# Kernel tuning notes

Measured on AMD Instinct MI355X. Metric: run time of the kernel, lower is better.

Reference implementation:

```python
import jax, jax.numpy as jnp
import numpy as np

B, C, H, W = 4, 16, 512, 512
OUT = 16
HID = 64
EPS = 1e-5


def _ln(x, g, b):
    mu = x.mean(-1, keepdims=True)
    v = x.var(-1, keepdims=True)
    return (x - mu) / jnp.sqrt(v + EPS) * g + b


def setup_inputs() -> dict:
    key = jax.random.key(0)
    ks = jax.random.split(key, 8)
    HW = H * W
    d = {}
    d['input'] = jax.random.normal(ks[0], (B, C, H, W), jnp.float32)
    d['W1'] = jax.random.normal(ks[1], (HID, HW), jnp.float32) * 0.01   # Linear1 weight [64, HW]
    d['b1'] = jnp.zeros((HID,), jnp.float32)
    d['ln1_g'] = jnp.ones((HID,), jnp.float32)
    d['ln1_b'] = jnp.zeros((HID,), jnp.float32)
    d['W2'] = jax.random.normal(ks[2], (HW, HID), jnp.float32) * 0.02   # Linear2 weight [HW, 64]
    d['b2'] = jnp.zeros((HW,), jnp.float32)
    d['ln2_g'] = jnp.ones((HW,), jnp.float32)
    d['ln2_b'] = jnp.zeros((HW,), jnp.float32)
    d['cw1'] = jax.random.normal(ks[3], (1, C, 1, 1), jnp.float32) * 0.1   # 1x1 conv C->1
    d['cb1'] = jnp.zeros((1,), jnp.float32)
    d['cw3'] = jax.random.normal(ks[4], (OUT, C, 3, 3), jnp.float32) * 0.05  # 3x3 conv C->OUT
    d['cb3'] = jnp.zeros((OUT,), jnp.float32)
    d['bn_g'] = jnp.ones((OUT,), jnp.float32)
    d['bn_b'] = jnp.zeros((OUT,), jnp.float32)
    return d


def reference(input, W1, b1, ln1_g, ln1_b, W2, b2, ln2_g, ln2_b, cw1, cb1, cw3, cb3, bn_g, bn_b):
    Bq, Cq, Hq, Wq = input.shape
    HW = Hq * Wq
    m = input.reshape(Bq, Cq, HW)
    # Linear1 -> LN -> ReLU  (per-channel over flattened spatial dim)
    h = jax.nn.relu(_ln(m @ W1.T + b1, ln1_g, ln1_b))            # [B, C, 64]
    # Linear2 -> LN -> ReLU
    m2 = jax.nn.relu(_ln(h @ W2.T + b2, ln2_g, ln2_b))           # [B, C, HW]
    m2 = m2.reshape(Bq, Cq, Hq, Wq)
    # 1x1 conv C -> 1
    score = jnp.einsum('bchw,oc->bohw', m2, cw1[:, :, 0, 0]) + cb1[:, None, None]  # [B,1,H,W]
    # keep_topk: ratio 0.25, no grad
    K = HW // 4
    flat = jax.lax.stop_gradient(score.reshape(Bq, HW))
    _, idx = jax.lax.top_k(flat, K)                               # [B, K]
    mask = jnp.zeros_like(flat).at[jnp.arange(Bq)[:, None], idx].set(1.0).reshape(Bq, 1, Hq, Wq)
    # boolean-mask gather: torch selects in ascending flat-index order
    idx_s = jnp.sort(idx, axis=1)                                 # [B, K]
    g = jnp.take_along_axis(m, idx_s[:, None, :], axis=2).reshape(Bq, Cq, Hq // 2, Wq // 2)
    # out_conv: 3x3 conv -> BatchNorm (batch stats, training mode) -> ReLU
    y = jax.lax.conv_general_dilated(g, cw3, (1, 1), [(1, 1), (1, 1)],
                                     dimension_numbers=('NCHW', 'OIHW', 'NCHW'))
    y = y + cb3[:, None, None]
    mu = y.mean((0, 2, 3), keepdims=True)
    v = y.var((0, 2, 3), keepdims=True)
    y = jax.nn.relu((y - mu) / jnp.sqrt(v + EPS) * bn_g[:, None, None] + bn_b[:, None, None])
    return (y, mask)
```

## Files before the change

### kernel.cpp

```cpp
#include <hip/hip_runtime.h>

#define HWN    262144
#define KSEL   65536
#define TIECAP 2048

#define OFF_H      0
#define OFF_DOT1   32768
#define OFF_G      65536
#define OFF_WBAR   98304
#define OFF_WB     98816
#define OFF_SB     99328
#define OFF_MU2    99360
#define OFF_ISIG2  99872
#define OFF_STATE  100384
#define OFF_HIST   100448
#define OFF_TIECNT 116832
#define OFF_CHCNT  116848
#define OFF_TIELST 116864
#define OFF_CHLST  149632
#define OFF_BCNT   182400
#define OFF_BOFF   186496
#define OFF_BNP    190592
#define OFF_BNC    452736
#define OFF_PART2  458752
#define OFF_HT     1015808
#define REGION2    1048576

__device__ __forceinline__ unsigned monokey(double s){
  unsigned long long b = (unsigned long long)__double_as_longlong(s);
  b = (b & 0x8000000000000000ULL) ? ~b : (b | 0x8000000000000000ULL);
  return (unsigned)(b >> 32);
}

__global__ void k_zero(unsigned* hist, unsigned* tiecnt, unsigned* chcnt, unsigned* state){
  int t = threadIdx.x;
  for (int i = t; i < 4096; i += 256) hist[i] = 0u;
  if (t < 4){
    tiecnt[t] = 0u; chcnt[t] = 0u;
    state[t*4+0] = 0u;
    state[t*4+1] = (unsigned)KSEL;
    state[t*4+2] = 0u;
    state[t*4+3] = 0u;
  }
}

__global__ __launch_bounds__(256) void k_gram(const float* __restrict__ W2,
                                              const float* __restrict__ b2,
                                              double* __restrict__ part, int subPerBlk){
  __shared__ float tile[64*68];
  __shared__ float b2t[64];
  int t = threadIdx.x, blk = blockIdx.x;
  int kt = t & 15, lt = t >> 4;
  double acc[16];
#pragma unroll
  for (int i=0;i<16;i++) acc[i]=0.0;
  double wbar4[4] = {0,0,0,0}, wb4[4] = {0,0,0,0};
  double sb = 0.0, sb2 = 0.0;
  int sub0 = blk * subPerBlk;
  for (int s = 0; s < subPerBlk; s++){
    int p0 = (sub0 + s) * 64;
#pragma unroll
    for (int i=0;i<4;i++){
      int j = t + 256*i;
      float4 v = ((const float4*)(W2 + (size_t)p0*64))[j];
      int e = j*4; int r = e >> 6; int c = e & 63;
      *((float4*)&tile[r*68 + c]) = v;
    }
    if (t < 64) b2t[t] = b2[p0 + t];
    __syncthreads();
    for (int r = 0; r < 64; r++){
      float4 k4 = *((const float4*)&tile[r*68 + kt*4]);
      float4 l4 = *((const float4*)&tile[r*68 + lt*4]);
      double k0=k4.x,k1=k4.y,k2=k4.z,k3=k4.w;
      double l0=l4.x,l1=l4.y,l2=l4.z,l3=l4.w;
      acc[0]+=k0*l0; acc[1]+=k0*l1; acc[2]+=k0*l2; acc[3]+=k0*l3;
      acc[4]+=k1*l0; acc[5]+=k1*l1; acc[6]+=k1*l2; acc[7]+=k1*l3;
      acc[8]+=k2*l0; acc[9]+=k2*l1; acc[10]+=k2*l2; acc[11]+=k2*l3;
      acc[12]+=k3*l0; acc[13]+=k3*l1; acc[14]+=k3*l2; acc[15]+=k3*l3;
      if (lt == 0){
        double bb = (double)b2t[r];
        wbar4[0]+=k0; wbar4[1]+=k1; wbar4[2]+=k2; wbar4[3]+=k3;
        wb4[0]+=k0*bb; wb4[1]+=k1*bb; wb4[2]+=k2*bb; wb4[3]+=k3*bb;
      }
      if (t == 0){ double bb=(double)b2t[r]; sb += bb; sb2 += bb*bb; }
    }
    __syncthreads();
  }
  double* pb = part + (size_t)blk * 4352;
#pragma unroll
  for (int i=0;i<4;i++)
#pragma unroll
    for (int j=0;j<4;j++)
      pb[(kt*4+i)*64 + (lt*4+j)] = acc[i*4+j];
  if (lt == 0){
#pragma unroll
    for (int i=0;i<4;i++){ pb[4096 + kt*4+i] = wbar4[i]; pb[4160 + kt*4+i] = wb4[i]; }
  }
  if (t == 0){ pb[4224]=sb; pb[4225]=sb2; }
}

__global__ __launch_bounds__(256) void k_red1(const double* __restrict__ part,
                                              double* __restrict__ part2, int bPerGrp){
  int jc = blockIdx.x % 17;
  int grp = blockIdx.x / 17;
  int j = jc*256 + threadIdx.x;
  const double* p = part + (size_t)grp * bPerGrp * 4352 + j;
  double s0=0.0, s1=0.0, s2=0.0, s3=0.0;
  for (int b = 0; b < bPerGrp; b += 4){
    s0 += p[(size_t)(b+0)*4352];
    s1 += p[(size_t)(b+1)*4352];
    s2 += p[(size_t)(b+2)*4352];
    s3 += p[(size_t)(b+3)*4352];
  }
  part2[(size_t)grp*4352 + j] = (s0+s1) + (s2+s3);
}

__global__ void k_redgram2(const double* __restrict__ part2,
                           double* __restrict__ G, double* __restrict__ wbar,
                           double* __restrict__ wb, double* __restrict__ sbv){
  int j = blockIdx.x*256 + threadIdx.x;
  if (j >= 4226) return;
  double s = 0.0;
#pragma unroll
  for (int b = 0; b < 16; b++) s += part2[(size_t)b*4352 + j];
  if (j < 4096) G[j] = s;
  else if (j < 4160) wbar[j-4096] = s;
  else if (j < 4224) wb[j-4160] = s;
  else sbv[j-4224] = s;
}

__global__ void k_reddot2(const double* __restrict__ part2, double* __restrict__ dot1){
  int j = blockIdx.x*256 + threadIdx.x;
  if (j >= 4096) return;
  double s = 0.0;
#pragma unroll
  for (int b = 0; b < 16; b++) s += part2[(size_t)b*4352 + j];
  dot1[j] = s;
}

__global__ __launch_bounds__(256) void k_gemm1(const float* __restrict__ inp,
                                               const float* __restrict__ W1,
                                               double* __restrict__ part, int subPerBlk){
  __shared__ float tm[64*72];
  __shared__ float tw[64*72];
  int t = threadIdx.x, blk = blockIdx.x;
  int rt = t & 15, kt = t >> 4;
  int rr = t >> 2, qi = t & 3;
  double acc[16];
#pragma unroll
  for (int i=0;i<16;i++) acc[i]=0.0;
  int sub0 = blk * subPerBlk;
  for (int s = 0; s < subPerBlk; s++){
    int p0 = (sub0 + s) * 64;
#pragma unroll
    for (int i=0;i<4;i++){
      int c = qi*16 + i*4;
      float4 v = *((const float4*)(inp + (size_t)rr*HWN + p0 + c));
      tm[(c+0)*72+rr]=v.x; tm[(c+1)*72+rr]=v.y; tm[(c+2)*72+rr]=v.z; tm[(c+3)*72+rr]=v.w;
      float4 w = *((const float4*)(W1 + (size_t)rr*HWN + p0 + c));
      tw[(c+0)*72+rr]=w.x; tw[(c+1)*72+rr]=w.y; tw[(c+2)*72+rr]=w.z; tw[(c+3)*72+rr]=w.w;
    }
    __syncthreads();
    for (int p = 0; p < 64; p++){
      float4 mv = *((const float4*)&tm[p*72 + rt*4]);
      float4 wv = *((const float4*)&tw[p*72 + kt*4]);
      double m0=mv.x,m1=mv.y,m2=mv.z,m3=mv.w;
      double w0=wv.x,w1=wv.y,w2=wv.z,w3=wv.w;
      acc[0]+=m0*w0; acc[1]+=m0*w1; acc[2]+=m0*w2; acc[3]+=m0*w3;
      acc[4]+=m1*w0; acc[5]+=m1*w1; acc[6]+=m1*w2; acc[7]+=m1*w3;
      acc[8]+=m2*w0; acc[9]+=m2*w1; acc[10]+=m2*w2; acc[11]+=m2*w3;
      acc[12]+=m3*w0; acc[13]+=m3*w1; acc[14]+=m3*w2; acc[15]+=m3*w3;
    }
    __syncthreads();
  }
  double* pb = part + (size_t)blk * 4352;
#pragma unroll
  for (int i=0;i<4;i++)
#pragma unroll
    for (int j=0;j<4;j++)
      pb[(rt*4+i)*64 + (kt*4+j)] = acc[i*4+j];
}

__global__ void k_h(const double* __restrict__ dot1, const float* __restrict__ b1,
                    const float* __restrict__ g1, const float* __restrict__ b1l,
                    const double* __restrict__ wbar, const double* __restrict__ sbv,
                    double* __restrict__ h, double* __restrict__ hT,
                    double* __restrict__ mu2){
  int r = threadIdx.x;
  double m = 0.0;
  for (int k=0;k<64;k++) m += dot1[r*64+k] + (double)b1[k];
  m *= (1.0/64.0);
  double v = 0.0;
  for (int k=0;k<64;k++){ double d = dot1[r*64+k] + (double)b1[k] - m; v += d*d; }
  v *= (1.0/64.0);
  double inv = 1.0 / sqrt(v + 1e-5);
  double s2 = 0.0;
  for (int k=0;k<64;k++){
    double x = dot1[r*64+k] + (double)b1[k];
    double z = (x - m) * inv;
    double hv = z * (double)g1[k] + (double)b1l[k];
    hv = hv > 0.0 ? hv : 0.0;
    h[r*64+k] = hv;
    hT[k*64+r] = hv;
    s2 += hv * wbar[k];
  }
  mu2[r] = (s2 + sbv[0]) / (double)HWN;
}

__global__ void k_var2(const double* __restrict__ h, const double* __restrict__ G,
                       const double* __restrict__ wb, const double* __restrict__ sbv,
                       const double* __restrict__ mu2, double* __restrict__ isig2){
  int r = blockIdx.x, k = threadIdx.x;
  double hk = h[r*64+k];
  double v = 0.0;
  for (int l=0;l<64;l++) v += G[k*64+l] * h[r*64+l];
  double contrib = hk*v + 2.0*hk*wb[k];
  for (int o=32;o>0;o>>=1) contrib += __shfl_down(contrib, o);
  if (k == 0){
    double E2 = (contrib + sbv[1]) / (double)HWN;
    double mu = mu2[r];
    double var = E2 - mu*mu;
    isig2[r] = 1.0 / sqrt(var + 1e-5);
  }
}

#define SC_K(WF, KIDX) { \
  double w_ = (double)(WF); \
  const double* hp_ = hb + (KIDX)*64; \
  acc[0]+=hp_[0]*w_;  acc[1]+=hp_[1]*w_;  acc[2]+=hp_[2]*w_;  acc[3]+=hp_[3]*w_; \
  acc[4]+=hp_[4]*w_;  acc[5]+=hp_[5]*w_;  acc[6]+=hp_[6]*w_;  acc[7]+=hp_[7]*w_; \
  acc[8]+=hp_[8]*w_;  acc[9]+=hp_[9]*w_;  acc[10]+=hp_[10]*w_; acc[11]+=hp_[11]*w_; \
  acc[12]+=hp_[12]*w_; acc[13]+=hp_[13]*w_; acc[14]+=hp_[14]*w_; acc[15]+=hp_[15]*w_; }

__global__ __launch_bounds__(256) void k_score(const float* __restrict__ W2,
    const float* __restrict__ b2, const float* __restrict__ g2, const float* __restrict__ lb2,
    const float* __restrict__ cw1, const float* __restrict__ cb1,
    const double* __restrict__ hT, const double* __restrict__ mu2, const double* __restrict__ isg,
    double* __restrict__ score, unsigned* __restrict__ key){
  int t = threadIdx.x;
  int p = blockIdx.x*256 + t;
  float4 w4[16];
  const float4* wp = (const float4*)(W2 + (size_t)p*64);
#pragma unroll
  for (int i=0;i<16;i++) w4[i] = wp[i];
  double g2p = (double)g2[p], lb2p = (double)lb2[p], b2p = (double)b2[p];
  double cb = (double)cb1[0];
  for (int b = 0; b < 4; b++){
    double acc[16];
#pragma unroll
    for (int j=0;j<16;j++) acc[j]=0.0;
    const double* hb = hT + b*16;
#pragma unroll
    for (int k4=0;k4<16;k4++){
      float4 wv = w4[k4];
      SC_K(wv.x, (k4*4+0))
      SC_K(wv.y, (k4*4+1))
      SC_K(wv.z, (k4*4+2))
      SC_K(wv.w, (k4*4+3))
    }
    double sc = cb;
#pragma unroll
    for (int j=0;j<16;j++){
      int c = b*16 + j;
      double tv = acc[j] + b2p;
      double z = (tv - mu2[c]) * isg[c];
      double v = z * g2p + lb2p;
      v = v > 0.0 ? v : 0.0;
      sc += v * (double)cw1[j];
    }
    if (sc == 0.0) sc = 0.0;
    score[(size_t)b*HWN + p] = sc;
    key[(size_t)b*HWN + p] = monokey(sc);
  }
}

__global__ void k_hist(const unsigned* __restrict__ key, const unsigned* __restrict__ state,
                       unsigned* __restrict__ hist, int pass){
  __shared__ unsigned lh[256];
  int t = threadIdx.x;
  int b = blockIdx.x >> 7, seg = blockIdx.x & 127;
  lh[t] = 0u;
  __syncthreads();
  unsigned pref = state[b*4+0];
  const unsigned* kb = key + (size_t)b*HWN + seg*2048;
  int shb = 24 - 8*pass;
#pragma unroll
  for (int i=0;i<8;i++){
    unsigned kk = kb[t + 256*i];
    bool ok = (pass == 0) || ((kk >> (32 - 8*pass)) == pref);
    if (ok) atomicAdd(&lh[(kk >> shb) & 255u], 1u);
  }
  __syncthreads();
  atomicAdd(&hist[(pass*4 + b)*256 + t], lh[t]);
}

__global__ void k_scan(unsigned* __restrict__ state, const unsigned* __restrict__ hist, int pass){
  __shared__ unsigned ls[4*256];
  int t = threadIdx.x;
  int b = t >> 8, j = t & 255;
  unsigned cnt = hist[(pass*4 + b)*256 + j];
  int q = 255 - j;
  ls[b*256 + q] = cnt;
  __syncthreads();
  for (int o=1;o<256;o<<=1){
    unsigned v = (q >= o) ? ls[b*256 + q - o] : 0u;
    __syncthreads();
    ls[b*256 + q] += v;
    __syncthreads();
  }
  unsigned need = state[b*4+1];
  unsigned pref = state[b*4+0];
  unsigned GT = (j == 255) ? 0u : ls[b*256 + (254 - j)];
  unsigned GE = ls[b*256 + (255 - j)];
  if (GT < need && need <= GE){
    unsigned npref = (pref << 8) | (unsigned)j;
    state[b*4+0] = npref;
    state[b*4+1] = need - GT;
    if (pass == 3){ state[b*4+2] = npref; state[b*4+3] = need - GT; }
  }
}

__global__ __launch_bounds__(256) void k_mask(const unsigned* __restrict__ key,
    const unsigned* __restrict__ state, float* __restrict__ outM,
    unsigned* __restrict__ bcnt, unsigned* __restrict__ tiecnt, unsigned* __restrict__ tielist){
  __shared__ int red[256];
  int t = threadIdx.x;
  int b = blockIdx.x >> 8, seg = blockIdx.x & 255;
  unsigned T = state[b*4+2];
  int p0 = seg*1024 + t*4;
  size_t base = (size_t)b*HWN + p0;
  uint4 kk = *((const uint4*)(key + base));
  float4 mv; int cnt = 0;
  { int s = kk.x > T; mv.x = s ? 1.f : 0.f; cnt += s;
    if (kk.x == T){ unsigned ti = atomicAdd(&tiecnt[b],1u); if (ti < TIECAP) tielist[b*TIECAP+ti] = (unsigned)(p0+0); } }
  { int s = kk.y > T; mv.y = s ? 1.f : 0.f; cnt += s;
    if (kk.y == T){ unsigned ti = atomicAdd(&tiecnt[b],1u); if (ti < TIECAP) tielist[b*TIECAP+ti] = (unsigned)(p0+1); } }
  { int s = kk.z > T; mv.z = s ? 1.f : 0.f; cnt += s;
    if (kk.z == T){ unsigned ti = atomicAdd(&tiecnt[b],1u); if (ti < TIECAP) tielist[b*TIECAP+ti] = (unsigned)(p0+2); } }
  { int s = kk.w > T; mv.w = s ? 1.f : 0.f; cnt += s;
    if (kk.w == T){ unsigned ti = atomicAdd(&tiecnt[b],1u); if (ti < TIECAP) tielist[b*TIECAP+ti] = (unsigned)(p0+3); } }
  *((float4*)(outM + base)) = mv;
  red[t] = cnt;
  __syncthreads();
  for (int o=128;o>0;o>>=1){ if (t < o) red[t] += red[t+o]; __syncthreads(); }
  if (t == 0) bcnt[b*256 + seg] = (unsigned)red[0];
}

__global__ __launch_bounds__(256) void k_ties(const unsigned* __restrict__ state,
    const unsigned* __restrict__ tiecnt, const unsigned* __restrict__ tielist,
    const double* __restrict__ score, float* __restrict__ outM,
    unsigned* __restrict__ chcnt, unsigned* __restrict__ chlist){
  __shared__ double ssc[TIECAP];
  __shared__ unsigned spp[TIECAP];
  __shared__ unsigned skeep[TIECAP];
  int b = blockIdx.x, t = threadIdx.x;
  unsigned tc = tiecnt[b];
  int n = (int)(tc < (unsigned)TIECAP ? tc : (unsigned)TIECAP);
  unsigned nt = state[b*4+3];
  for (int i=t;i<n;i+=256){
    unsigned p = tielist[b*TIECAP+i];
    spp[i] = p; ssc[i] = score[(size_t)b*HWN + p];
  }
  __syncthreads();
  for (int i=t;i<n;i+=256){
    double si = ssc[i]; unsigned pi = spp[i]; int r = 0;
    for (int j=0;j<n;j++){
      double sj = ssc[j]; unsigned pj = spp[j];
      if (sj > si || (sj == si && pj < pi)) r++;
    }
    skeep[i] = (r < (int)nt) ? 1u : 0u;
  }
  __syncthreads();
  for (int i=t;i<n;i+=256){
    if (skeep[i]){
      unsigned pi = spp[i]; int r2 = 0;
      for (int j=0;j<n;j++) if (skeep[j] && spp[j] < pi) r2++;
      chlist[b*TIECAP + r2] = pi;
      outM[(size_t)b*HWN + pi] = 1.0f;
    }
  }
  if (t == 0){
    unsigned c = ((unsigned)n < nt) ? (unsigned)n : nt;
    chcnt[b] = c;
  }
}

__global__ void k_scanblk(const unsigned* __restrict__ bcnt, unsigned* __restrict__ boff){
  __shared__ unsigned ls[1024];
  int t = threadIdx.x; int b = t >> 8, j = t & 255;
  unsigned own = bcnt[b*256 + j];
  ls[t] = own;
  __syncthreads();
  for (int o=1;o<256;o<<=1){
    unsigned v = (j >= o) ? ls[b*256 + j - o] : 0u;
    __syncthreads();
    ls[t] += v;
    __syncthreads();
  }
  boff[b*256 + j] = ls[t] - own;
}

__device__ __forceinline__ void gath_one(unsigned kv, int p, unsigned T,
    const unsigned* __restrict__ cl, unsigned nch, unsigned base, int& run,
    const float* __restrict__ inp, float* __restrict__ g, int b){
  int isGT = kv > T;
  int isCh = 0;
  if (kv == T && nch > 0u){
    for (unsigned j=0;j<nch;j++) if (cl[j] == (unsigned)p){ isCh = 1; break; }
  }
  if (isGT | isCh){
    unsigned adj = 0;
    for (unsigned j=0;j<nch;j++) adj += (cl[j] < (unsigned)p) ? 1u : 0u;
    unsigned rank = base + (unsigned)run + adj;
#pragma unroll
    for (int c=0;c<16;c++)
      g[(size_t)(b*16+c)*KSEL + rank] = inp[(size_t)(b*16+c)*HWN + p];
  }
  run += isGT;
}

__global__ __launch_bounds__(256) void k_gather(const unsigned* __restrict__ key,
    const unsigned* __restrict__ state, const unsigned* __restrict__ boff,
    const unsigned* __restrict__ chcnt, const unsigned* __restrict__ chlist,
    const float* __restrict__ inp, float* __restrict__ g){
  __shared__ int wt[4];
  int t = threadIdx.x;
  int b = blockIdx.x >> 8, seg = blockIdx.x & 255;
  unsigned T = state[b*4+2];
  int p0 = seg*1024 + t*4;
  uint4 kk = *((const uint4*)(key + (size_t)b*HWN + p0));
  int s0 = kk.x > T, s1 = kk.y > T, s2 = kk.z > T, s3 = kk.w > T;
  int cnt = s0 + s1 + s2 + s3;
  int l = t & 63;
  int incl = cnt;
#pragma unroll
  for (int o=1;o<64;o<<=1){ int v = __shfl_up(incl, o); if (l >= o) incl += v; }
  int w = t >> 6;
  if (l == 63) wt[w] = incl;
  __syncthreads();
  int wex = 0;
#pragma unroll
  for (int i=0;i<4;i++) if (i < w) wex += wt[i];
  int exth = incl - cnt;
  unsigned base = boff[b*256 + seg] + (unsigned)wex + (unsigned)exth;
  unsigned nch = chcnt[b];
  const unsigned* cl = chlist + b*TIECAP;
  int run = 0;
  gath_one(kk.x, p0+0, T, cl, nch, base, run, inp, g, b);
  gath_one(kk.y, p0+1, T, cl, nch, base, run, inp, g, b);
  gath_one(kk.z, p0+2, T, cl, nch, base, run, inp, g, b);
  gath_one(kk.w, p0+3, T, cl, nch, base, run, inp, g, b);
}

__global__ __launch_bounds__(256) void k_conv(const float* __restrict__ g,
    const float* __restrict__ cw3, const float* __restrict__ cb3,
    float* __restrict__ outY, double* __restrict__ bnp){
  __shared__ float wsm[2304];
  __shared__ float it[18*18];
  __shared__ double red[16][4][2];
  int t = threadIdx.x;
  int b = blockIdx.x >> 8, tile = blockIdx.x & 255;
  int ty0 = (tile >> 4) * 16, tx0 = (tile & 15) * 16;
  int tx = t & 15, ty = t >> 4;
#pragma unroll
  for (int i=0;i<9;i++){ int j = t + 256*i; if (j < 2304) wsm[j] = cw3[j]; }
  float acc[16];
#pragma unroll
  for (int i=0;i<16;i++) acc[i] = 0.f;
  for (int ic=0; ic<16; ic++){
    __syncthreads();
    for (int j=t;j<324;j+=256){
      int gy = ty0 - 1 + j/18, gx = tx0 - 1 + (j%18);
      float v = 0.f;
      if (gy >= 0 && gy < 256 && gx >= 0 && gx < 256)
        v = g[(size_t)(b*16+ic)*KSEL + gy*256 + gx];
      it[j] = v;
    }
    __syncthreads();
#pragma unroll
    for (int ky=0;ky<3;ky++)
#pragma unroll
      for (int kx=0;kx<3;kx++){
        float v = it[(ty+ky)*18 + tx+kx];
#pragma unroll
        for (int oc=0;oc<16;oc++) acc[oc] += v * wsm[oc*144 + ic*9 + ky*3 + kx];
      }
  }
  int w = t >> 6, l = t & 63;
  for (int oc=0;oc<16;oc++){
    float yv = acc[oc] + cb3[oc];
    outY[(size_t)(b*16+oc)*KSEL + (ty0+ty)*256 + tx0+tx] = yv;
    double s = (double)yv, q = (double)yv*(double)yv;
    for (int o=32;o>0;o>>=1){ s += __shfl_down(s, o); q += __shfl_down(q, o); }
    if (l == 0){ red[oc][w][0] = s; red[oc][w][1] = q; }
  }
  __syncthreads();
  if (t < 16){
    double s=0.0, q=0.0;
    for (int w2=0;w2<4;w2++){ s += red[t][w2][0]; q += red[t][w2][1]; }
    bnp[(size_t)blockIdx.x*32 + t*2]   = s;
    bnp[(size_t)blockIdx.x*32 + t*2+1] = q;
  }
}

__global__ void k_bnred(const double* __restrict__ bnp, const float* __restrict__ bng,
                        const float* __restrict__ bnb, float* __restrict__ bnc){
  __shared__ double red[16][16][2];
  int t = threadIdx.x; int oc = t >> 4, sl = t & 15;
  double s = 0.0, q = 0.0;
  for (int i=0;i<64;i++){
    int blk = sl*64 + i;
    s += bnp[(size_t)blk*32 + oc*2];
    q += bnp[(size_t)blk*32 + oc*2+1];
  }
  red[oc][sl][0] = s; red[oc][sl][1] = q;
  __syncthreads();
  if (t < 16){
    double S=0.0, Q=0.0;
    for (int i=0;i<16;i++){ S += red[t][i][0]; Q += red[t][i][1]; }
    double N = 262144.0;
    double mu = S/N, var = Q/N - mu*mu;
    double inv = 1.0 / sqrt(var + 1e-5);
    double a = (double)bng[t] * inv;
    double bsh = (double)bnb[t] - mu*a;
    bnc[t*2] = (float)a; bnc[t*2+1] = (float)bsh;
  }
}

__global__ void k_bnapply(float* __restrict__ outY, const float* __restrict__ bnc){
  int i = blockIdx.x*256 + threadIdx.x;
  float4 v = ((float4*)outY)[i];
  int oc = (i >> 14) & 15;
  float a = bnc[oc*2], bsh = bnc[oc*2+1];
  v.x = fmaxf(v.x*a + bsh, 0.f);
  v.y = fmaxf(v.y*a + bsh, 0.f);
  v.z = fmaxf(v.z*a + bsh, 0.f);
  v.w = fmaxf(v.w*a + bsh, 0.f);
  ((float4*)outY)[i] = v;
}

extern "C" void kernel_launch(void* const* d_in, const int* in_sizes, int n_in,
                              void* d_out, int out_size, void* d_ws, size_t ws_size,
                              hipStream_t stream){
  const float* inp  = (const float*)d_in[0];
  const float* W1   = (const float*)d_in[1];
  const float* b1   = (const float*)d_in[2];
  const float* g1   = (const float*)d_in[3];
  const float* b1l  = (const float*)d_in[4];
  const float* W2   = (const float*)d_in[5];
  const float* b2   = (const float*)d_in[6];
  const float* g2   = (const float*)d_in[7];
  const float* lb2  = (const float*)d_in[8];
  const float* cw1  = (const float*)d_in[9];
  const float* cb1  = (const float*)d_in[10];
  const float* cw3  = (const float*)d_in[11];
  const float* cb3  = (const float*)d_in[12];
  const float* bng  = (const float*)d_in[13];
  const float* bnb  = (const float*)d_in[14];
  (void)in_sizes; (void)n_in; (void)out_size;

  char* ws = (char*)d_ws;
  float* outY = (float*)d_out;
  float* outM = outY + 4194304;

  int NB;
  size_t need512 = (size_t)REGION2 + 512ull*4352*8 + 16777216ull;
  size_t need128 = (size_t)REGION2 + 12582912ull + 16777216ull;
  if (ws_size >= need512) NB = 512;
  else if (ws_size >= need128) NB = 128;
  else NB = 64;
  size_t partBytes = (size_t)NB * 4352 * 8;
  size_t gbufOff = (size_t)REGION2 + (partBytes > 12582912ull ? partBytes : 12582912ull);
  int subPerBlk = 4096 / NB;
  int bPerGrp = NB / 16;

  double*  part   = (double*)(ws + REGION2);
  double*  score  = (double*)(ws + REGION2);
  unsigned* key   = (unsigned*)(ws + REGION2 + 8388608ull);
  float*   gbuf   = (float*)(ws + gbufOff);
  double*  hbuf   = (double*)(ws + OFF_H);
  double*  hTbuf  = (double*)(ws + OFF_HT);
  double*  dot1   = (double*)(ws + OFF_DOT1);
  double*  G      = (double*)(ws + OFF_G);
  double*  wbar   = (double*)(ws + OFF_WBAR);
  double*  wb     = (double*)(ws + OFF_WB);
  double*  sbv    = (double*)(ws + OFF_SB);
  double*  mu2    = (double*)(ws + OFF_MU2);
  double*  isg    = (double*)(ws + OFF_ISIG2);
  unsigned* state = (unsigned*)(ws + OFF_STATE);
  unsigned* hist  = (unsigned*)(ws + OFF_HIST);
  unsigned* tiecnt= (unsigned*)(ws + OFF_TIECNT);
  unsigned* chcnt = (unsigned*)(ws + OFF_CHCNT);
  unsigned* tielist=(unsigned*)(ws + OFF_TIELST);
  unsigned* chlist= (unsigned*)(ws + OFF_CHLST);
  unsigned* bcnt  = (unsigned*)(ws + OFF_BCNT);
  unsigned* boff  = (unsigned*)(ws + OFF_BOFF);
  double*  bnp    = (double*)(ws + OFF_BNP);
  float*   bnc    = (float*)(ws + OFF_BNC);
  double*  part2  = (double*)(ws + OFF_PART2);

  k_zero<<<1, 256, 0, stream>>>(hist, tiecnt, chcnt, state);
  k_gram<<<NB, 256, 0, stream>>>(W2, b2, part, subPerBlk);
  k_red1<<<17*16, 256, 0, stream>>>(part, part2, bPerGrp);
  k_redgram2<<<17, 256, 0, stream>>>(part2, G, wbar, wb, sbv);
  k_gemm1<<<NB, 256, 0, stream>>>(inp, W1, part, subPerBlk);
  k_red1<<<17*16, 256, 0, stream>>>(part, part2, bPerGrp);
  k_reddot2<<<16, 256, 0, stream>>>(part2, dot1);
  k_h<<<1, 64, 0, stream>>>(dot1, b1, g1, b1l, wbar, sbv, hbuf, hTbuf, mu2);
  k_var2<<<64, 64, 0, stream>>>(hbuf, G, wb, sbv, mu2, isg);
  k_score<<<1024, 256, 0, stream>>>(W2, b2, g2, lb2, cw1, cb1, hTbuf, mu2, isg, score, key);
  for (int pass = 0; pass < 4; pass++){
    k_hist<<<512, 256, 0, stream>>>(key, state, hist, pass);
    k_scan<<<1, 1024, 0, stream>>>(state, hist, pass);
  }
  k_mask<<<1024, 256, 0, stream>>>(key, state, outM, bcnt, tiecnt, tielist);
  k_ties<<<4, 256, 0, stream>>>(state, tiecnt, tielist, score, outM, chcnt, chlist);
  k_scanblk<<<1, 1024, 0, stream>>>(bcnt, boff);
  k_gather<<<1024, 256, 0, stream>>>(key, state, boff, chcnt, chlist, inp, gbuf);
  k_conv<<<1024, 256, 0, stream>>>(gbuf, cw3, cb3, outY, bnp);
  k_bnred<<<1, 256, 0, stream>>>(bnp, bng, bnb, bnc);
  k_bnapply<<<4096, 256, 0, stream>>>(outY, bnc);
}
```

Before: 463.2 us.

## Use FP64 MFMA for the Gram and first GEMM partial reductions

Rewrites k_gram and k_gemm1 to use the fp64 16x16x4 MFMA matrix instructions in place of scalar double FMAs staged through shared memory. The bias row and a ones row are folded into an extra MFMA, so the b2 products and sums come out of the same pass, and the partial-buffer stride is tightened to 4226 and 4096 elements. The aim is to cut the FP64 ALU cost of these two large reductions over HW. It adds lane-to-output index mapping via probe MFMAs, which is subtle and could misplace results.

```diff
diff --git a/kernel.cpp b/kernel.cpp
--- a/kernel.cpp
+++ b/kernel.cpp
@@ -26,6 +26,12 @@
 #define OFF_HT     1015808
 #define REGION2    1048576
 
+#define PS_GRAM 4226
+#define PS_DOT  4096
+
+typedef double d4_t __attribute__((ext_vector_type(4)));
+typedef float  f4v  __attribute__((ext_vector_type(4)));
+
 __device__ __forceinline__ unsigned monokey(double s){
   unsigned long long b = (unsigned long long)__double_as_longlong(s);
   b = (b & 0x8000000000000000ULL) ? ~b : (b | 0x8000000000000000ULL);
@@ -46,139 +52,142 @@
 
 __global__ __launch_bounds__(256) void k_gram(const float* __restrict__ W2,
                                               const float* __restrict__ b2,
-                                              double* __restrict__ part, int subPerBlk){
-  __shared__ float tile[64*68];
-  __shared__ float b2t[64];
-  int t = threadIdx.x, blk = blockIdx.x;
-  int kt = t & 15, lt = t >> 4;
-  double acc[16];
-#pragma unroll
-  for (int i=0;i<16;i++) acc[i]=0.0;
-  double wbar4[4] = {0,0,0,0}, wb4[4] = {0,0,0,0};
-  double sb = 0.0, sb2 = 0.0;
-  int sub0 = blk * subPerBlk;
-  for (int s = 0; s < subPerBlk; s++){
-    int p0 = (sub0 + s) * 64;
-#pragma unroll
-    for (int i=0;i<4;i++){
-      int j = t + 256*i;
-      float4 v = ((const float4*)(W2 + (size_t)p0*64))[j];
-      int e = j*4; int r = e >> 6; int c = e & 63;
-      *((float4*)&tile[r*68 + c]) = v;
+                                              double* __restrict__ part, int pPerBlk){
+  int t = threadIdx.x;
+  int w = t >> 6, l = t & 63;
+  int q = l >> 4, m = l & 15;
+  int p0 = blockIdx.x * pPerBlk;
+  d4_t acc0 = {0.,0.,0.,0.}, acc1 = {0.,0.,0.,0.}, acc2 = {0.,0.,0.,0.};
+  d4_t acc3 = {0.,0.,0.,0.}, acc4 = {0.,0.,0.,0.}, acc44 = {0.,0.,0.,0.};
+  const float* base = W2 + (size_t)(p0 + q)*64 + m;
+  const float* b2p  = b2 + p0 + q;
+  int nCh = pPerBlk >> 2;
+  for (int c = 0; c < nCh; c++){
+    double f0 = (double)base[0];
+    double f1 = (double)base[16];
+    double f2 = (double)base[32];
+    double f3 = (double)base[48];
+    double bb = (double)b2p[0];
+    double f4 = (m == 0) ? bb : ((m == 1) ? 1.0 : 0.0);
+    double fa = (w == 0) ? f0 : ((w == 1) ? f1 : ((w == 2) ? f2 : f3));
+    acc0 = __builtin_amdgcn_mfma_f64_16x16x4f64(fa, f0, acc0, 0, 0, 0);
+    acc1 = __builtin_amdgcn_mfma_f64_16x16x4f64(fa, f1, acc1, 0, 0, 0);
+    acc2 = __builtin_amdgcn_mfma_f64_16x16x4f64(fa, f2, acc2, 0, 0, 0);
+    acc3 = __builtin_amdgcn_mfma_f64_16x16x4f64(fa, f3, acc3, 0, 0, 0);
+    acc4 = __builtin_amdgcn_mfma_f64_16x16x4f64(fa, f4, acc4, 0, 0, 0);
+    if (w == 0)
+      acc44 = __builtin_amdgcn_mfma_f64_16x16x4f64(f4, f4, acc44, 0, 0, 0);
+    base += 256; b2p += 4;
+  }
+  d4_t prD = {0.,0.,0.,0.}, pcD = {0.,0.,0.,0.};
+  double rp = (double)(1 + m);
+  prD = __builtin_amdgcn_mfma_f64_16x16x4f64(rp, 1.0, prD, 0, 0, 0);
+  pcD = __builtin_amdgcn_mfma_f64_16x16x4f64(1.0, rp, pcD, 0, 0, 0);
+  double* P = part + (size_t)blockIdx.x * PS_GRAM;
+#pragma unroll
+  for (int i = 0; i < 4; i++){
+    int ri = ((((int)prD[i]) >> 2) - 1) & 15;
+    int ci = ((((int)pcD[i]) >> 2) - 1) & 15;
+    int r = w*16 + ri;
+    P[r*66 +  0 + ci] = acc0[i];
+    P[r*66 + 16 + ci] = acc1[i];
+    P[r*66 + 32 + ci] = acc2[i];
+    P[r*66 + 48 + ci] = acc3[i];
+    if (ci < 2) P[r*66 + 64 + ci] = acc4[i];
+    if (w == 0 && ri == 0 && ci < 2) P[4224 + ci] = acc44[i];
+  }
+}
+
+__global__ __launch_bounds__(256) void k_gemm1(const float* __restrict__ inp,
+                                               const float* __restrict__ W1,
+                                               double* __restrict__ part, int pPerBlk){
+  int t = threadIdx.x;
+  int w = t >> 6, l = t & 63;
+  int q = l >> 4, m = l & 15;
+  int p0 = blockIdx.x * pPerBlk;
+  d4_t acc0 = {0.,0.,0.,0.}, acc1 = {0.,0.,0.,0.};
+  d4_t acc2 = {0.,0.,0.,0.}, acc3 = {0.,0.,0.,0.};
+  const f4v* ap  = (const f4v*)(inp + (size_t)(w*16 + m)*HWN + p0 + q*4);
+  const f4v* bp0 = (const f4v*)(W1  + (size_t)( 0 + m)*HWN + p0 + q*4);
+  const f4v* bp1 = (const f4v*)(W1  + (size_t)(16 + m)*HWN + p0 + q*4);
+  const f4v* bp2 = (const f4v*)(W1  + (size_t)(32 + m)*HWN + p0 + q*4);
+  const f4v* bp3 = (const f4v*)(W1  + (size_t)(48 + m)*HWN + p0 + q*4);
+  int nCh = pPerBlk >> 4;
+  for (int c = 0; c < nCh; c++){
+    f4v av = ap [(size_t)c*4];
+    f4v b0 = bp0[(size_t)c*4];
+    f4v b1 = bp1[(size_t)c*4];
+    f4v b2v= bp2[(size_t)c*4];
+    f4v b3 = bp3[(size_t)c*4];
+#pragma unroll
+    for (int t4 = 0; t4 < 4; t4++){
+      double a = (double)av[t4];
+      acc0 = __builtin_amdgcn_mfma_f64_16x16x4f64(a, (double)b0[t4],  acc0, 0, 0, 0);
+      acc1 = __builtin_amdgcn_mfma_f64_16x16x4f64(a, (double)b1[t4],  acc1, 0, 0, 0);
+      acc2 = __builtin_amdgcn_mfma_f64_16x16x4f64(a, (double)b2v[t4], acc2, 0, 0, 0);
+      acc3 = __builtin_amdgcn_mfma_f64_16x16x4f64(a, (double)b3[t4],  acc3, 0, 0, 0);
     }
-    if (t < 64) b2t[t] = b2[p0 + t];
-    __syncthreads();
-    for (int r = 0; r < 64; r++){
-      float4 k4 = *((const float4*)&tile[r*68 + kt*4]);
-      float4 l4 = *((const float4*)&tile[r*68 + lt*4]);
-      double k0=k4.x,k1=k4.y,k2=k4.z,k3=k4.w;
-      double l0=l4.x,l1=l4.y,l2=l4.z,l3=l4.w;
-      acc[0]+=k0*l0; acc[1]+=k0*l1; acc[2]+=k0*l2; acc[3]+=k0*l3;
-      acc[4]+=k1*l0; acc[5]+=k1*l1; acc[6]+=k1*l2; acc[7]+=k1*l3;
-      acc[8]+=k2*l0; acc[9]+=k2*l1; acc[10]+=k2*l2; acc[11]+=k2*l3;
-      acc[12]+=k3*l0; acc[13]+=k3*l1; acc[14]+=k3*l2; acc[15]+=k3*l3;
-      if (lt == 0){
-        double bb = (double)b2t[r];
-        wbar4[0]+=k0; wbar4[1]+=k1; wbar4[2]+=k2; wbar4[3]+=k3;
-        wb4[0]+=k0*bb; wb4[1]+=k1*bb; wb4[2]+=k2*bb; wb4[3]+=k3*bb;
-      }
-      if (t == 0){ double bb=(double)b2t[r]; sb += bb; sb2 += bb*bb; }
-    }
-    __syncthreads();
-  }
-  double* pb = part + (size_t)blk * 4352;
-#pragma unroll
-  for (int i=0;i<4;i++)
-#pragma unroll
-    for (int j=0;j<4;j++)
-      pb[(kt*4+i)*64 + (lt*4+j)] = acc[i*4+j];
-  if (lt == 0){
-#pragma unroll
-    for (int i=0;i<4;i++){ pb[4096 + kt*4+i] = wbar4[i]; pb[4160 + kt*4+i] = wb4[i]; }
-  }
-  if (t == 0){ pb[4224]=sb; pb[4225]=sb2; }
+  }
+  d4_t prD = {0.,0.,0.,0.}, pcD = {0.,0.,0.,0.};
+  double rp = (double)(1 + m);
+  prD = __builtin_amdgcn_mfma_f64_16x16x4f64(rp, 1.0, prD, 0, 0, 0);
+  pcD = __builtin_amdgcn_mfma_f64_16x16x4f64(1.0, rp, pcD, 0, 0, 0);
+  double* P = part + (size_t)blockIdx.x * PS_DOT;
+#pragma unroll
+  for (int i = 0; i < 4; i++){
+    int ri = ((((int)prD[i]) >> 2) - 1) & 15;
+    int ci = ((((int)pcD[i]) >> 2) - 1) & 15;
+    int r = w*16 + ri;
+    P[r*64 +  0 + ci] = acc0[i];
+    P[r*64 + 16 + ci] = acc1[i];
+    P[r*64 + 32 + ci] = acc2[i];
+    P[r*64 + 48 + ci] = acc3[i];
+  }
 }
 
 __global__ __launch_bounds__(256) void k_red1(const double* __restrict__ part,
-                                              double* __restrict__ part2, int bPerGrp){
-  int jc = blockIdx.x % 17;
-  int grp = blockIdx.x / 17;
+                                              double* __restrict__ part2,
+                                              int bPerGrp, int cnt){
+  int nj = (cnt + 255) >> 8;
+  int jc = blockIdx.x % nj;
+  int grp = blockIdx.x / nj;
   int j = jc*256 + threadIdx.x;
-  const double* p = part + (size_t)grp * bPerGrp * 4352 + j;
+  if (j >= cnt) return;
+  const double* p = part + (size_t)grp * bPerGrp * cnt + j;
   double s0=0.0, s1=0.0, s2=0.0, s3=0.0;
   for (int b = 0; b < bPerGrp; b += 4){
-    s0 += p[(size_t)(b+0)*4352];
-    s1 += p[(size_t)(b+1)*4352];
-    s2 += p[(size_t)(b+2)*4352];
-    s3 += p[(size_t)(b+3)*4352];
-  }
-  part2[(size_t)grp*4352 + j] = (s0+s1) + (s2+s3);
+    s0 += p[(size_t)(b+0)*cnt];
+    s1 += p[(size_t)(b+1)*cnt];
+    s2 += p[(size_t)(b+2)*cnt];
+    s3 += p[(size_t)(b+3)*cnt];
+  }
+  part2[(size_t)grp*cnt + j] = (s0+s1) + (s2+s3);
 }
 
 __global__ void k_redgram2(const double* __restrict__ part2,
-                           double* __restrict__ G, double* __restrict__ wbar,
-                           double* __restrict__ wb, double* __restrict__ sbv){
+                           double* __restrict__ G, double* __restrict__ wb,
+                           double* __restrict__ wbar, double* __restrict__ sbv){
   int j = blockIdx.x*256 + threadIdx.x;
-  if (j >= 4226) return;
+  if (j >= PS_GRAM) return;
   double s = 0.0;
 #pragma unroll
-  for (int b = 0; b < 16; b++) s += part2[(size_t)b*4352 + j];
-  if (j < 4096) G[j] = s;
-  else if (j < 4160) wbar[j-4096] = s;
-  else if (j < 4224) wb[j-4160] = s;
-  else sbv[j-4224] = s;
+  for (int b = 0; b < 16; b++) s += part2[(size_t)b*PS_GRAM + j];
+  if (j < 4224){
+    int r = j / 66, c = j % 66;
+    if (c < 64) G[r*64 + c] = s;
+    else if (c == 64) wb[r] = s;
+    else wbar[r] = s;
+  } else if (j == 4224) sbv[1] = s;
+  else sbv[0] = s;
 }
 
 __global__ void k_reddot2(const double* __restrict__ part2, double* __restrict__ dot1){
   int j = blockIdx.x*256 + threadIdx.x;
-  if (j >= 4096) return;
+  if (j >= PS_DOT) return;
   double s = 0.0;
 #pragma unroll
-  for (int b = 0; b < 16; b++) s += part2[(size_t)b*4352 + j];
+  for (int b = 0; b < 16; b++) s += part2[(size_t)b*PS_DOT + j];
   dot1[j] = s;
-}
-
-__global__ __launch_bounds__(256) void k_gemm1(const float* __restrict__ inp,
-                                               const float* __restrict__ W1,
-                                               double* __restrict__ part, int subPerBlk){
-  __shared__ float tm[64*72];
-  __shared__ float tw[64*72];
-  int t = threadIdx.x, blk = blockIdx.x;
-  int rt = t & 15, kt = t >> 4;
-  int rr = t >> 2, qi = t & 3;
-  double acc[16];
-#pragma unroll
-  for (int i=0;i<16;i++) acc[i]=0.0;
-  int sub0 = blk * subPerBlk;
-  for (int s = 0; s < subPerBlk; s++){
-    int p0 = (sub0 + s) * 64;
-#pragma unroll
-    for (int i=0;i<4;i++){
-      int c = qi*16 + i*4;
-      float4 v = *((const float4*)(inp + (size_t)rr*HWN + p0 + c));
-      tm[(c+0)*72+rr]=v.x; tm[(c+1)*72+rr]=v.y; tm[(c+2)*72+rr]=v.z; tm[(c+3)*72+rr]=v.w;
-      float4 w = *((const float4*)(W1 + (size_t)rr*HWN + p0 + c));
-      tw[(c+0)*72+rr]=w.x; tw[(c+1)*72+rr]=w.y; tw[(c+2)*72+rr]=w.z; tw[(c+3)*72+rr]=w.w;
-    }
-    __syncthreads();
-    for (int p = 0; p < 64; p++){
-      float4 mv = *((const float4*)&tm[p*72 + rt*4]);
-      float4 wv = *((const float4*)&tw[p*72 + kt*4]);
-      double m0=mv.x,m1=mv.y,m2=mv.z,m3=mv.w;
-      double w0=wv.x,w1=wv.y,w2=wv.z,w3=wv.w;
-      acc[0]+=m0*w0; acc[1]+=m0*w1; acc[2]+=m0*w2; acc[3]+=m0*w3;
-      acc[4]+=m1*w0; acc[5]+=m1*w1; acc[6]+=m1*w2; acc[7]+=m1*w3;
-      acc[8]+=m2*w0; acc[9]+=m2*w1; acc[10]+=m2*w2; acc[11]+=m2*w3;
-      acc[12]+=m3*w0; acc[13]+=m3*w1; acc[14]+=m3*w2; acc[15]+=m3*w3;
-    }
-    __syncthreads();
-  }
-  double* pb = part + (size_t)blk * 4352;
-#pragma unroll
-  for (int i=0;i<4;i++)
-#pragma unroll
-    for (int j=0;j<4;j++)
-      pb[(rt*4+i)*64 + (kt*4+j)] = acc[i*4+j];
 }
 
 __global__ void k_h(const double* __restrict__ dot1, const float* __restrict__ b1,
@@ -571,7 +580,7 @@
   else NB = 64;
   size_t partBytes = (size_t)NB * 4352 * 8;
   size_t gbufOff = (size_t)REGION2 + (partBytes > 12582912ull ? partBytes : 12582912ull);
-  int subPerBlk = 4096 / NB;
+  int pPerBlk = HWN / NB;
   int bPerGrp = NB / 16;
 
   double*  part   = (double*)(ws + REGION2);
@@ -600,11 +609,11 @@
   double*  part2  = (double*)(ws + OFF_PART2);
 
   k_zero<<<1, 256, 0, stream>>>(hist, tiecnt, chcnt, state);
-  k_gram<<<NB, 256, 0, stream>>>(W2, b2, part, subPerBlk);
-  k_red1<<<17*16, 256, 0, stream>>>(part, part2, bPerGrp);
-  k_redgram2<<<17, 256, 0, stream>>>(part2, G, wbar, wb, sbv);
-  k_gemm1<<<NB, 256, 0, stream>>>(inp, W1, part, subPerBlk);
-  k_red1<<<17*16, 256, 0, stream>>>(part, part2, bPerGrp);
+  k_gram<<<NB, 256, 0, stream>>>(W2, b2, part, pPerBlk);
+  k_red1<<<17*16, 256, 0, stream>>>(part, part2, bPerGrp, PS_GRAM);
+  k_redgram2<<<17, 256, 0, stream>>>(part2, G, wb, wbar, sbv);
+  k_gemm1<<<NB, 256, 0, stream>>>(inp, W1, part, pPerBlk);
+  k_red1<<<16*16, 256, 0, stream>>>(part, part2, bPerGrp, PS_DOT);
   k_reddot2<<<16, 256, 0, stream>>>(part2, dot1);
   k_h<<<1, 64, 0, stream>>>(dot1, b1, g1, b1l, wbar, sbv, hbuf, hTbuf, mu2);
   k_var2<<<64, 64, 0, stream>>>(hbuf, G, wb, sbv, mu2, isg);
```

Result: faster. 424.2 us (-8.4%).
